# Performance work log

Hardware: AMD Instinct MI355X
Metric: run time of the kernel (lower is better)

Reference implementation:

```python
import jax, jax.numpy as jnp
import numpy as np

FP8_MAX = 448.0  # e4m3 max
SCALE_MARGIN = 0.8


def _fp8_quant_dequant(t, scale):
    # scaled value is <= 448*0.8 by construction, so no saturation/overflow
    q = (t / scale).astype(jnp.float8_e4m3fn)
    return q.astype(jnp.float32) * scale


def setup_inputs() -> dict:
    key = jax.random.key(0)
    k1, k2 = jax.random.split(key)
    B, S, D_IN, D_OUT = 4, 2048, 2048, 2048
    x = jax.random.normal(k1, (B, S, D_IN), dtype=jnp.float32)
    weight = jax.random.normal(k2, (D_OUT, D_IN), dtype=jnp.float32)
    bias = jnp.zeros((D_OUT,), dtype=jnp.float32)
    return {"x": x, "weight": weight, "bias": bias}


def reference(x, weight, bias):
    # Shared FP8ScalingManager: amax history = [amax_x] for x, then [amax_x, amax_w] for w.
    amax_x = jnp.max(jnp.abs(x))
    amax_w = jnp.max(jnp.abs(weight))
    x_scale = amax_x / (FP8_MAX * SCALE_MARGIN)
    w_scale = jnp.maximum(amax_x, amax_w) / (FP8_MAX * SCALE_MARGIN)  # history max
    x_scale = jax.lax.stop_gradient(x_scale)  # .item() detaches in torch
    w_scale = jax.lax.stop_gradient(w_scale)
    # quantize to fp8 e4m3, dequantize, scaled matmul (math of torch._scaled_mm)
    x_dq = _fp8_quant_dequant(x, x_scale)      # [B,S,Din]
    w_dq = _fp8_quant_dequant(weight, w_scale)  # [Dout,Din]
    out = jnp.einsum('bsd,od->bso', x_dq, w_dq)  # [B,S,Dout]
    return out + bias
```

## Files before the change

kernel.cpp:

```cpp
#include <hip/hip_runtime.h>
#include <stdint.h>

typedef float v4f __attribute__((ext_vector_type(4)));
typedef int v8i __attribute__((ext_vector_type(8)));

#define FP8_DENOM 358.4f


__device__ __forceinline__ unsigned pack4_fp8(float a, float b, float c, float d) {
  int v = 0;
  v = __builtin_amdgcn_cvt_pk_fp8_f32(a, b, v, false);
  v = __builtin_amdgcn_cvt_pk_fp8_f32(c, d, v, true);
  return (unsigned)v;
}

__device__ __forceinline__ void gload_lds16(const void* g, void* l) {
  __builtin_amdgcn_global_load_lds(
      (const __attribute__((address_space(1))) uint32_t*)(uintptr_t)g,
      (__attribute__((address_space(3))) uint32_t*)(uint32_t)(uintptr_t)l,
      16, 0, 0);
}


__global__ void __launch_bounds__(256) amax_part(const float4* __restrict__ x,
                                                 const float4* __restrict__ w,
                                                 float* __restrict__ part) {
  const int b = blockIdx.x, t = threadIdx.x;
  const float4* p = (b < 1024) ? x : w;
  const long base = (long)((b < 1024) ? b : (b - 1024)) * 4096;
  float m0 = 0.f, m1 = 0.f, m2 = 0.f, m3 = 0.f;
#pragma unroll
  for (int j = 0; j < 4; ++j) {
    float4 v0 = p[base + (j * 4 + 0) * 256 + t];
    float4 v1 = p[base + (j * 4 + 1) * 256 + t];
    float4 v2 = p[base + (j * 4 + 2) * 256 + t];
    float4 v3 = p[base + (j * 4 + 3) * 256 + t];
    m0 = fmaxf(m0, fmaxf(fmaxf(fabsf(v0.x), fabsf(v0.y)), fmaxf(fabsf(v0.z), fabsf(v0.w))));
    m1 = fmaxf(m1, fmaxf(fmaxf(fabsf(v1.x), fabsf(v1.y)), fmaxf(fabsf(v1.z), fabsf(v1.w))));
    m2 = fmaxf(m2, fmaxf(fmaxf(fabsf(v2.x), fabsf(v2.y)), fmaxf(fabsf(v2.z), fabsf(v2.w))));
    m3 = fmaxf(m3, fmaxf(fmaxf(fabsf(v3.x), fabsf(v3.y)), fmaxf(fabsf(v3.z), fabsf(v3.w))));
  }
  float m = fmaxf(fmaxf(m0, m1), fmaxf(m2, m3));
#pragma unroll
  for (int off = 32; off > 0; off >>= 1)
    m = fmaxf(m, __shfl_down(m, off, 64));
  __shared__ float red[4];
  const int lane = t & 63, wvid = t >> 6;
  if (lane == 0) red[wvid] = m;
  __syncthreads();
  if (t == 0) part[b] = fmaxf(fmaxf(red[0], red[1]), fmaxf(red[2], red[3]));
}


__global__ void __launch_bounds__(256) scale_reduce(const float* __restrict__ part,
                                                    unsigned* __restrict__ amax) {
  const int t = threadIdx.x;
  float mx = fmaxf(fmaxf(part[t], part[t + 256]), fmaxf(part[t + 512], part[t + 768]));
  float mw = part[1024 + t];
#pragma unroll
  for (int off = 32; off > 0; off >>= 1) {
    mx = fmaxf(mx, __shfl_down(mx, off, 64));
    mw = fmaxf(mw, __shfl_down(mw, off, 64));
  }
  __shared__ float rx[4], rw[4];
  const int lane = t & 63, wvid = t >> 6;
  if (lane == 0) { rx[wvid] = mx; rw[wvid] = mw; }
  __syncthreads();
  if (t == 0) {
    amax[0] = __float_as_uint(fmaxf(fmaxf(rx[0], rx[1]), fmaxf(rx[2], rx[3])));
    amax[1] = __float_as_uint(fmaxf(fmaxf(rw[0], rw[1]), fmaxf(rw[2], rw[3])));
  }
}


__global__ void quant2_kernel(const float4* __restrict__ x, uint4* __restrict__ xq, int nx16,
                              const float4* __restrict__ w, uint4* __restrict__ wq, int nw16,
                              int xblocks, const unsigned* __restrict__ amax) {
  const float ax = __uint_as_float(amax[0]);
  const float aw = __uint_as_float(amax[1]);
  const int isw = ((int)blockIdx.x >= xblocks) ? 1 : 0;
  const float scale = isw ? (fmaxf(ax, aw) / FP8_DENOM) : (ax / FP8_DENOM);
  const float4* in = isw ? w : x;
  uint4* outq = isw ? wq : xq;
  const int n16 = isw ? nw16 : nx16;
  const int b0 = isw ? ((int)blockIdx.x - xblocks) : (int)blockIdx.x;
  const int nb = isw ? ((int)gridDim.x - xblocks) : xblocks;
  const long stride = (long)nb * blockDim.x;
  for (long i = (long)b0 * blockDim.x + threadIdx.x; i < n16; i += stride) {
    float4 v0 = in[4 * i + 0], v1 = in[4 * i + 1], v2 = in[4 * i + 2], v3 = in[4 * i + 3];
    uint4 r;
    r.x = pack4_fp8(v0.x / scale, v0.y / scale, v0.z / scale, v0.w / scale);
    r.y = pack4_fp8(v1.x / scale, v1.y / scale, v1.z / scale, v1.w / scale);
    r.z = pack4_fp8(v2.x / scale, v2.y / scale, v2.z / scale, v2.w / scale);
    r.w = pack4_fp8(v3.x / scale, v3.y / scale, v3.z / scale, v3.w / scale);
    outq[i] = r;
  }
}


__global__ void __launch_bounds__(256) gemm_mx(
    const uint8_t* __restrict__ Aq, const uint8_t* __restrict__ Bq,
    const float* __restrict__ bias, float* __restrict__ out,
    const unsigned* __restrict__ amax) {
  constexpr int K = 2048, N = 2048, BK = 128;
  __shared__ alignas(16) uint8_t sA[128 * BK];
  __shared__ alignas(16) uint8_t sB[128 * BK];

  const int tid = threadIdx.x;
  const int lane = tid & 63;
  const int wid = tid >> 6;
  const int wy = wid >> 1, wx = wid & 1;
  const long tileM = (long)blockIdx.y * 128;
  const long tileN = (long)blockIdx.x * 128;

  v4f acc[4][4];
#pragma unroll
  for (int i = 0; i < 4; ++i)
#pragma unroll
    for (int j = 0; j < 4; ++j) acc[i][j] = (v4f)(0.f);

  const int srow = tid >> 3;
  const int schunk = (tid & 7) ^ (srow & 7);
  const uint8_t* gA = Aq + (tileM + srow) * K + schunk * 16;
  const uint8_t* gB = Bq + (tileN + srow) * K + schunk * 16;

  const int q = lane >> 4;
  const int mrow = lane & 15;

  int aoff[4][2], boff[4][2];
#pragma unroll
  for (int i = 0; i < 4; ++i) {
    const int rA = wy * 64 + i * 16 + mrow, swA = rA & 7;
    aoff[i][0] = rA * 128 + 16 * ((2 * q) ^ swA);
    aoff[i][1] = rA * 128 + 16 * ((2 * q + 1) ^ swA);
    const int rB = wx * 64 + i * 16 + mrow, swB = rB & 7;
    boff[i][0] = rB * 128 + 16 * ((2 * q) ^ swB);
    boff[i][1] = rB * 128 + 16 * ((2 * q + 1) ^ swB);
  }

  for (int k0 = 0; k0 < K; k0 += BK) {
#pragma unroll
    for (int s = 0; s < 4; ++s) {
      gload_lds16(gA + (long)s * 32 * K + k0, sA + s * 4096 + tid * 16);
      gload_lds16(gB + (long)s * 32 * K + k0, sB + s * 4096 + tid * 16);
    }
    __syncthreads();

    union Frag { v8i v; uint4 h[2]; };
    Frag a[4], b[4];
#pragma unroll
    for (int i = 0; i < 4; ++i) {
      a[i].h[0] = *(const uint4*)(sA + aoff[i][0]);
      a[i].h[1] = *(const uint4*)(sA + aoff[i][1]);
      b[i].h[0] = *(const uint4*)(sB + boff[i][0]);
      b[i].h[1] = *(const uint4*)(sB + boff[i][1]);
    }
#pragma unroll
    for (int i = 0; i < 4; ++i)
#pragma unroll
      for (int j = 0; j < 4; ++j)
        acc[i][j] = __builtin_amdgcn_mfma_scale_f32_16x16x128_f8f6f4(
            a[i].v, b[j].v, acc[i][j],  0,  0,
             0, 0x7F7F7F7F,  0, 0x7F7F7F7F);
    __syncthreads();
  }

  const float ax = __uint_as_float(amax[0]);
  const float aw = __uint_as_float(amax[1]);
  const float scale = (ax / FP8_DENOM) * (fmaxf(ax, aw) / FP8_DENOM);
#pragma unroll
  for (int j = 0; j < 4; ++j) {
    const long col = tileN + wx * 64 + j * 16 + mrow;
    const float bv = bias[col];
#pragma unroll
    for (int i = 0; i < 4; ++i) {
      const long row = tileM + wy * 64 + i * 16 + q * 4;
#pragma unroll
      for (int r = 0; r < 4; ++r)
        out[(row + r) * N + col] = acc[i][j][r] * scale + bv;
    }
  }
}


extern "C" void kernel_launch(void* const* d_in, const int* in_sizes, int n_in,
                              void* d_out, int out_size, void* d_ws, size_t ws_size,
                              hipStream_t stream) {
  const float* x = (const float*)d_in[0];
  const float* w = (const float*)d_in[1];
  const float* bias = (const float*)d_in[2];
  float* out = (float*)d_out;

  const int M = 8192, N = 2048, K = 2048;
  const long nx = (long)M * K, nw = (long)N * K;

  unsigned* amax = (unsigned*)d_ws;
  float* part = (float*)((uint8_t*)d_ws + 256);
  uint8_t* xq = (uint8_t*)d_ws + 8192;
  uint8_t* wq = xq + nx;

  amax_part<<<1280, 256, 0, stream>>>((const float4*)x, (const float4*)w, part);
  scale_reduce<<<1, 256, 0, stream>>>(part, amax);
  quant2_kernel<<<5120, 256, 0, stream>>>((const float4*)x, (uint4*)xq, (int)(nx / 16),
                                          (const float4*)w, (uint4*)wq, (int)(nw / 16),
                                          4096, amax);
  gemm_mx<<<dim3(N / 128, M / 128), 256, 0, stream>>>(xq, wq, bias, out, amax);
}
```

Before: 179.6 us.

## Double-buffer GEMM LDS tiles and precompute reciprocal quantization scales

The FP8 GEMM main loop now uses two LDS buffers per operand. The next K-tile's global-to-LDS loads are issued right after a single barrier, so they overlap the MFMA work on the current tile, and the loop needs one barrier per iteration instead of two. The scale-reduce kernel also precomputes the reciprocal scales and the combined output scale, so the quantize kernel multiplies instead of dividing and the epilogue loads one value. The trade-offs are that doubling LDS per block may lower occupancy, and multiplying by a reciprocal can change FP8 rounding in rare edge cases.

```diff
diff --git a/kernel.cpp b/kernel.cpp
--- a/kernel.cpp
+++ b/kernel.cpp
@@ -67,8 +67,15 @@
   if (lane == 0) { rx[wvid] = mx; rw[wvid] = mw; }
   __syncthreads();
   if (t == 0) {
-    amax[0] = __float_as_uint(fmaxf(fmaxf(rx[0], rx[1]), fmaxf(rx[2], rx[3])));
-    amax[1] = __float_as_uint(fmaxf(fmaxf(rw[0], rw[1]), fmaxf(rw[2], rw[3])));
+    const float ax = fmaxf(fmaxf(rx[0], rx[1]), fmaxf(rx[2], rx[3]));
+    const float aw = fmaxf(fmaxf(rw[0], rw[1]), fmaxf(rw[2], rw[3]));
+    const float sx = ax / FP8_DENOM;
+    const float sw = fmaxf(ax, aw) / FP8_DENOM;
+    amax[0] = __float_as_uint(ax);
+    amax[1] = __float_as_uint(aw);
+    amax[2] = __float_as_uint(1.0f / sx);
+    amax[3] = __float_as_uint(1.0f / sw);
+    amax[4] = __float_as_uint(sx * sw);
   }
 }
 
@@ -76,10 +83,8 @@
 __global__ void quant2_kernel(const float4* __restrict__ x, uint4* __restrict__ xq, int nx16,
                               const float4* __restrict__ w, uint4* __restrict__ wq, int nw16,
                               int xblocks, const unsigned* __restrict__ amax) {
-  const float ax = __uint_as_float(amax[0]);
-  const float aw = __uint_as_float(amax[1]);
   const int isw = ((int)blockIdx.x >= xblocks) ? 1 : 0;
-  const float scale = isw ? (fmaxf(ax, aw) / FP8_DENOM) : (ax / FP8_DENOM);
+  const float rs = __uint_as_float(amax[2 + isw]);
   const float4* in = isw ? w : x;
   uint4* outq = isw ? wq : xq;
   const int n16 = isw ? nw16 : nx16;
@@ -89,10 +94,10 @@
   for (long i = (long)b0 * blockDim.x + threadIdx.x; i < n16; i += stride) {
     float4 v0 = in[4 * i + 0], v1 = in[4 * i + 1], v2 = in[4 * i + 2], v3 = in[4 * i + 3];
     uint4 r;
-    r.x = pack4_fp8(v0.x / scale, v0.y / scale, v0.z / scale, v0.w / scale);
-    r.y = pack4_fp8(v1.x / scale, v1.y / scale, v1.z / scale, v1.w / scale);
-    r.z = pack4_fp8(v2.x / scale, v2.y / scale, v2.z / scale, v2.w / scale);
-    r.w = pack4_fp8(v3.x / scale, v3.y / scale, v3.z / scale, v3.w / scale);
+    r.x = pack4_fp8(v0.x * rs, v0.y * rs, v0.z * rs, v0.w * rs);
+    r.y = pack4_fp8(v1.x * rs, v1.y * rs, v1.z * rs, v1.w * rs);
+    r.z = pack4_fp8(v2.x * rs, v2.y * rs, v2.z * rs, v2.w * rs);
+    r.w = pack4_fp8(v3.x * rs, v3.y * rs, v3.z * rs, v3.w * rs);
     outq[i] = r;
   }
 }
@@ -102,9 +107,9 @@
     const uint8_t* __restrict__ Aq, const uint8_t* __restrict__ Bq,
     const float* __restrict__ bias, float* __restrict__ out,
     const unsigned* __restrict__ amax) {
-  constexpr int K = 2048, N = 2048, BK = 128;
-  __shared__ alignas(16) uint8_t sA[128 * BK];
-  __shared__ alignas(16) uint8_t sB[128 * BK];
+  constexpr int K = 2048, N = 2048, BK = 128, ITERS = K / BK;
+  __shared__ alignas(16) uint8_t sA[2][128 * BK];
+  __shared__ alignas(16) uint8_t sB[2][128 * BK];
 
   const int tid = threadIdx.x;
   const int lane = tid & 63;
@@ -138,22 +143,29 @@
     boff[i][1] = rB * 128 + 16 * ((2 * q + 1) ^ swB);
   }
 
-  for (int k0 = 0; k0 < K; k0 += BK) {
+  auto stage = [&](int buf, int k0) {
 #pragma unroll
     for (int s = 0; s < 4; ++s) {
-      gload_lds16(gA + (long)s * 32 * K + k0, sA + s * 4096 + tid * 16);
-      gload_lds16(gB + (long)s * 32 * K + k0, sB + s * 4096 + tid * 16);
+      gload_lds16(gA + (long)s * 32 * K + k0, &sA[buf][s * 4096 + tid * 16]);
+      gload_lds16(gB + (long)s * 32 * K + k0, &sB[buf][s * 4096 + tid * 16]);
     }
+  };
+
+  stage(0, 0);
+  for (int it = 0; it < ITERS; ++it) {
     __syncthreads();
-
+    if (it + 1 < ITERS) stage((it + 1) & 1, (it + 1) * BK);
+
+    const uint8_t* bufA = sA[it & 1];
+    const uint8_t* bufB = sB[it & 1];
     union Frag { v8i v; uint4 h[2]; };
     Frag a[4], b[4];
 #pragma unroll
     for (int i = 0; i < 4; ++i) {
-      a[i].h[0] = *(const uint4*)(sA + aoff[i][0]);
-      a[i].h[1] = *(const uint4*)(sA + aoff[i][1]);
-      b[i].h[0] = *(const uint4*)(sB + boff[i][0]);
-      b[i].h[1] = *(const uint4*)(sB + boff[i][1]);
+      a[i].h[0] = *(const uint4*)(bufA + aoff[i][0]);
+      a[i].h[1] = *(const uint4*)(bufA + aoff[i][1]);
+      b[i].h[0] = *(const uint4*)(bufB + boff[i][0]);
+      b[i].h[1] = *(const uint4*)(bufB + boff[i][1]);
     }
 #pragma unroll
     for (int i = 0; i < 4; ++i)
@@ -162,12 +174,9 @@
         acc[i][j] = __builtin_amdgcn_mfma_scale_f32_16x16x128_f8f6f4(
             a[i].v, b[j].v, acc[i][j],  0,  0,
              0, 0x7F7F7F7F,  0, 0x7F7F7F7F);
-    __syncthreads();
-  }
-
-  const float ax = __uint_as_float(amax[0]);
-  const float aw = __uint_as_float(amax[1]);
-  const float scale = (ax / FP8_DENOM) * (fmaxf(ax, aw) / FP8_DENOM);
+  }
+
+  const float scale = __uint_as_float(amax[4]);
 #pragma unroll
   for (int j = 0; j < 4; ++j) {
     const long col = tileN + wx * 64 + j * 16 + mrow;
```

Result: no change. 176.5 us (-1.8%).
